# Kernel optimization log

Hardware: AMD Instinct MI355X
Metric: run time of the kernel (lower is better)

## Reference

```python
import jax, jax.numpy as jnp
import numpy as np
import math

B, N, W = 8, 2048, 512

def setup_inputs() -> dict:
    key0 = jax.random.key(0)
    ks = jax.random.split(key0, 6)
    return {
        "query": jax.random.normal(ks[0], (B, N, W), dtype=jnp.float32),
        "key":   jax.random.normal(ks[1], (B, N, W), dtype=jnp.float32),
        "W1": jax.random.normal(ks[2], (W, W), dtype=jnp.float32) * (1.0 / math.sqrt(W)),
        "b1": jax.random.normal(ks[3], (W,), dtype=jnp.float32) * 0.01,
        "W2": jax.random.normal(ks[4], (W, W), dtype=jnp.float32) * (1.0 / math.sqrt(W)),
        "b2": jax.random.normal(ks[5], (W,), dtype=jnp.float32) * 0.01,
    }

def _attn(q, k, v):
    # scores: [B, N, N]
    d_k = q.shape[-1]
    scores = jnp.einsum('bnd,bmd->bnm', q, k) / jnp.sqrt(jnp.asarray(d_k, q.dtype))
    p = jax.nn.softmax(scores, axis=-1)
    return jnp.einsum('bnm,bmd->bnd', p, v)

def reference(query, key, W1, b1, W2, b2):
    # nn.Linear: x @ W.T + b
    q = jnp.einsum('bnd,ed->bne', query, W1) + b1
    k = jnp.einsum('bnd,ed->bne', key, W2) + b2
    x1 = _attn(q, k, q)  # attention(query, key, query)
    x2 = _attn(k, q, k)  # attention(key, query, key)
    return jnp.concatenate((x1, x2), axis=1)  # [B, 2N, W]
```

## Files before the change

kernel.cpp:

```cpp
#include <hip/hip_runtime.h>
#include <hip/hip_bf16.h>
#include <stdint.h>

typedef unsigned short ushort_t;
typedef __attribute__((ext_vector_type(8))) short short8;
typedef __attribute__((ext_vector_type(4))) short short4v;
typedef __attribute__((ext_vector_type(4))) float f32x4;

__device__ inline ushort_t f2bf(float x) {
  uint32_t u = __float_as_uint(x);
  u += 0x7fffu + ((u >> 16) & 1u);
  return (ushort_t)(u >> 16);
}
__device__ inline float bfu2f(uint32_t h) { return __uint_as_float(h << 16); }

__device__ inline uint32_t pk2bf(float a, float b) {
  __hip_bfloat162 h = __float22bfloat162_rn(make_float2(a, b));
  union { __hip_bfloat162 h2; uint32_t u; } cv; cv.h2 = h; return cv.u;
}

__device__ inline void gload_lds16(const void* g, void* l) {
  __builtin_amdgcn_global_load_lds((const __attribute__((address_space(1))) uint32_t*)g,
                                   (__attribute__((address_space(3))) uint32_t*)l, 16, 0, 0);
}

__global__ __launch_bounds__(512, 4) void linear_kernel(
    const float* __restrict__ query, const float* __restrict__ key,
    const float* __restrict__ W1, const float* __restrict__ b1,
    const float* __restrict__ W2, const float* __restrict__ b2,
    ushort_t* __restrict__ q_bf, ushort_t* __restrict__ k_bf,
    ushort_t* __restrict__ qT, ushort_t* __restrict__ kT)
{
  extern __shared__ __attribute__((aligned(16))) ushort_t smL[];

  int bx = blockIdx.x;
  int which = bx & 1, rt = bx >> 1;
  const float* X    = which ? key : query;
  const float* Wm   = which ? W2  : W1;
  const float* bias = which ? b2  : b1;
  ushort_t* OUT  = which ? k_bf : q_bf;
  ushort_t* OUTT = which ? kT   : qT;

  int t = threadIdx.x, w = t >> 6, lane = t & 63, g = lane >> 4, m = lane & 15;

  {
    int tp = t & 127, rsub = t >> 7;
#pragma unroll 4
    for (int p = 0; p < 16; ++p) {
      int row = p * 4 + rsub;
      f32x4 v = *(const f32x4*)(X + (size_t)(rt * 64 + row) * 512 + tp * 4);
      uint2 dv;
      dv.x = pk2bf(v[0], v[1]);
      dv.y = pk2bf(v[2], v[3]);
      int chunk = tp >> 1;
      int phys = chunk ^ (row & 7);
      *(uint2*)&smL[row * 512 + phys * 8 + (tp & 1) * 4] = dv;
    }
  }
  __syncthreads();

  f32x4 zero = {0.f, 0.f, 0.f, 0.f};
  f32x4 acc[4][4];
#pragma unroll
  for (int i = 0; i < 4; ++i)
#pragma unroll
    for (int j = 0; j < 4; ++j) acc[i][j] = zero;

  const float* Wbase = Wm + (size_t)(w * 64) * 512;

  for (int k0 = 0; k0 < 16; ++k0) {
    short8 bfr[4];
#pragma unroll
    for (int j = 0; j < 4; ++j) {
      const float* wp = Wbase + (size_t)(16 * j + m) * 512 + k0 * 32 + g * 8;
      f32x4 lo = *(const f32x4*)wp;
      f32x4 hi = *(const f32x4*)(wp + 4);
      union { uint32_t u[4]; short8 s; } fb;
      fb.u[0] = pk2bf(lo[0], lo[1]); fb.u[1] = pk2bf(lo[2], lo[3]);
      fb.u[2] = pk2bf(hi[0], hi[1]); fb.u[3] = pk2bf(hi[2], hi[3]);
      bfr[j] = fb.s;
    }
    short8 afr[4];
#pragma unroll
    for (int i = 0; i < 4; ++i) {
      int row = 16 * i + m;
      int phys = (k0 * 4 + g) ^ (m & 7);
      afr[i] = *(const short8*)&smL[row * 512 + phys * 8];
    }
#pragma unroll
    for (int i = 0; i < 4; ++i)
#pragma unroll
      for (int j = 0; j < 4; ++j)
        acc[i][j] = __builtin_amdgcn_mfma_f32_16x16x32_bf16(afr[i], bfr[j], acc[i][j], 0, 0, 0);
  }

  float bw[4];
#pragma unroll
  for (int j = 0; j < 4; ++j) bw[j] = bias[w * 64 + 16 * j + m];

  __syncthreads();

#pragma unroll
  for (int j = 0; j < 4; ++j)
#pragma unroll
    for (int i = 0; i < 4; ++i) {
      f32x4 c4 = acc[i][j];
#pragma unroll
      for (int rr = 0; rr < 4; ++rr)
        smL[(16 * i + 4 * g + rr) * 520 + w * 64 + 16 * j + m] = f2bf(c4[rr] + bw[j]);
    }
  __syncthreads();
  {
    int row = t >> 3, oct = t & 7;
    size_t gb = (size_t)(rt * 64 + row) * 512 + oct * 64;
#pragma unroll
    for (int i2 = 0; i2 < 8; ++i2)
      *(short8*)(OUT + gb + i2 * 8) = *(const short8*)&smL[row * 520 + oct * 64 + i2 * 8];
  }
  __syncthreads();

#pragma unroll
  for (int j = 0; j < 4; ++j)
#pragma unroll
    for (int i = 0; i < 4; ++i) {
      f32x4 c4 = acc[i][j];
      short4v tv;
#pragma unroll
      for (int rr = 0; rr < 4; ++rr) tv[rr] = (short)f2bf(c4[rr] + bw[j]);
      *(short4v*)&smL[(w * 64 + 16 * j + m) * 68 + 16 * i + 4 * g] = tv;
    }
  __syncthreads();
  {
    size_t b_ = (size_t)(rt >> 5);
    size_t gb = b_ * (512 * 2048) + (size_t)t * 2048 + (size_t)(rt & 31) * 64;
#pragma unroll
    for (int i2 = 0; i2 < 8; ++i2)
      *(short8*)(OUTT + gb + i2 * 8) = *(const short8*)&smL[t * 68 + i2 * 8];
  }
}

__global__ __launch_bounds__(512, 2) void attn_kernel(
    const ushort_t* __restrict__ qb, const ushort_t* __restrict__ kb_,
    const ushort_t* __restrict__ qT, const ushort_t* __restrict__ kT,
    float* __restrict__ out)
{
  extern __shared__ ushort_t sm[];
  const float CEXP = 1.4426950408889634f / 22.62741699796952f;

  int bx = blockIdx.x;
  int group = bx & 15, mtile = bx >> 4;
  int b = group >> 1, att = group & 1;
  const ushort_t* Qp = (att ? kb_ : qb) + (size_t)b * (2048 * 512);
  const ushort_t* Kp = (att ? qb  : kb_) + (size_t)b * (2048 * 512);
  const ushort_t* Vt = (att ? kT  : qT)  + (size_t)b * (512 * 2048);

  int t = threadIdx.x, w = t >> 6, lane = t & 63, g = lane >> 4, m = lane & 15;
  int dq = w >> 1, qh = w & 1;
  int qrow = mtile * 128 + w * 16 + m;
  int sw8  = ((g ^ ((m >> 1) & 3)) * 8);
  int srow = lane >> 2;
  int soff = ((lane & 3) ^ ((lane >> 3) & 3)) * 8;
  int pm6 = (m & 6);

  ushort_t* Plds = sm + 65536;
  float* lbuf = (float*)(sm + 69632);

  int pw0 = (w * 16 + m) * 32 + ((g ^ pm6) << 2);
  int pw1 = (w * 16 + m) * 32 + (((g + 4) ^ pm6) << 2);
  int prq[4];
#pragma unroll
  for (int qt = 0; qt < 4; ++qt)
    prq[qt] = (qh * 64 + qt * 16 + m) * 32 + (((2 * g) ^ pm6) << 2);

  short8 qf[16];
#pragma unroll
  for (int ks = 0; ks < 16; ++ks)
    qf[ks] = *(const short8*)(Qp + (size_t)qrow * 512 + ks * 32 + g * 8);

  f32x4 zero = {0.f, 0.f, 0.f, 0.f};
  f32x4 acc[8][4];
#pragma unroll
  for (int dt = 0; dt < 8; ++dt)
#pragma unroll
    for (int qt = 0; qt < 4; ++qt) acc[dt][qt] = zero;
  float l = 0.f;

  auto stage = [&](int buf, int kb) {
    ushort_t* base = sm + buf * 32768;
    const int kbase = kb * 32;
#pragma unroll
    for (int i = 0; i < 4; ++i) {
      int qi = w * 4 + i, ks = qi >> 1, tt2 = qi & 1;
      const ushort_t* gsrc = Kp + (size_t)(kbase + tt2 * 16 + srow) * 512 + ks * 32 + soff;
      gload_lds16(gsrc, base + ks * 1024 + tt2 * 512);
    }
#pragma unroll
    for (int i = 0; i < 4; ++i) {
      int qi = w * 4 + i;
      const ushort_t* gsrc = Vt + (size_t)(qi * 16 + srow) * 2048 + kbase + soff;
      gload_lds16(gsrc, base + 16384 + qi * 512);
    }
  };

  stage(0, 0);

  for (int kb = 0; kb < 64; ++kb) {
    int cur = kb & 1;
    __syncthreads();
    if (kb + 1 < 64) stage(1 - cur, kb + 1);
    const ushort_t* base = sm + cur * 32768;

    f32x4 T0 = zero, T1 = zero;
    __builtin_amdgcn_s_setprio(1);
#pragma unroll
    for (int ks = 0; ks < 16; ++ks) {
      short8 k0 = *(const short8*)&base[ks * 1024 +       m * 32 + sw8];
      short8 k1 = *(const short8*)&base[ks * 1024 + 512 + m * 32 + sw8];
      T0 = __builtin_amdgcn_mfma_f32_16x16x32_bf16(k0, qf[ks], T0, 0, 0, 0);
      T1 = __builtin_amdgcn_mfma_f32_16x16x32_bf16(k1, qf[ks], T1, 0, 0, 0);
    }
    __builtin_amdgcn_s_setprio(0);

    uint32_t h[8];
#pragma unroll
    for (int r = 0; r < 4; ++r) {
      float e0 = __builtin_amdgcn_exp2f(T0[r] * CEXP);
      float e1 = __builtin_amdgcn_exp2f(T1[r] * CEXP);
      h[r]     = f2bf(e0);
      h[4 + r] = f2bf(e1);
      l += bfu2f(h[r]) + bfu2f(h[4 + r]);
    }
    uint2 p0, p1;
    p0.x = h[0] | (h[1] << 16); p0.y = h[2] | (h[3] << 16);
    p1.x = h[4] | (h[5] << 16); p1.y = h[6] | (h[7] << 16);
    *(uint2*)&Plds[pw0] = p0;
    *(uint2*)&Plds[pw1] = p1;

    __syncthreads();

    short8 pf[4];
#pragma unroll
    for (int qt = 0; qt < 4; ++qt) pf[qt] = *(const short8*)&Plds[prq[qt]];
    __builtin_amdgcn_s_setprio(1);
#pragma unroll
    for (int dt = 0; dt < 8; ++dt) {
      short8 vf = *(const short8*)&base[16384 + (dq * 8 + dt) * 512 + m * 32 + sw8];
#pragma unroll
      for (int qt = 0; qt < 4; ++qt)
        acc[dt][qt] = __builtin_amdgcn_mfma_f32_16x16x32_bf16(vf, pf[qt], acc[dt][qt], 0, 0, 0);
    }
    __builtin_amdgcn_s_setprio(0);
  }

  l += __shfl_xor(l, 16, 64);
  l += __shfl_xor(l, 32, 64);
  if (lane < 16) lbuf[w * 16 + lane] = 1.0f / l;
  __syncthreads();

  float inv[4];
#pragma unroll
  for (int qt = 0; qt < 4; ++qt) inv[qt] = lbuf[qh * 64 + qt * 16 + m];
  size_t orow = (size_t)b * 4096 + (size_t)att * 2048 + mtile * 128 + qh * 64 + m;
#pragma unroll
  for (int qt = 0; qt < 4; ++qt) {
    float* ob = out + (orow + qt * 16) * 512 + dq * 128;
#pragma unroll
    for (int dt = 0; dt < 8; ++dt) {
      f32x4 v = acc[dt][qt] * inv[qt];
      *(f32x4*)(ob + dt * 16 + g * 4) = v;
    }
  }
}

extern "C" void kernel_launch(void* const* d_in, const int* in_sizes, int n_in,
                              void* d_out, int out_size, void* d_ws, size_t ws_size,
                              hipStream_t stream) {
  const float* query = (const float*)d_in[0];
  const float* key   = (const float*)d_in[1];
  const float* W1    = (const float*)d_in[2];
  const float* b1    = (const float*)d_in[3];
  const float* W2    = (const float*)d_in[4];
  const float* b2    = (const float*)d_in[5];
  float* out = (float*)d_out;

  ushort_t* ws   = (ushort_t*)d_ws;
  ushort_t* q_bf = ws;
  ushort_t* k_bf = ws + 8388608;
  ushort_t* qT   = ws + 16777216;
  ushort_t* kT   = ws + 25165824;

  (void)hipFuncSetAttribute((const void*)linear_kernel,
                            hipFuncAttributeMaxDynamicSharedMemorySize, 69632);
  (void)hipFuncSetAttribute((const void*)attn_kernel,
                            hipFuncAttributeMaxDynamicSharedMemorySize, 139776);

  linear_kernel<<<512, 512, 69632, stream>>>(query, key, W1, b1, W2, b2,
                                             q_bf, k_bf, qT, kT);
  attn_kernel<<<256, 512, 139776, stream>>>(q_bf, k_bf, qT, kT, out);
}
```

Baseline: 331.9 us.

## Pre-convert weights to bf16 and double linear-kernel row tile to 128

Adds a small kernel that converts W1/W2 to bf16 once, so the linear kernel loads bf16 weight fragments directly instead of converting fp32 weights inside every block. The linear kernel now processes 128 rows per block instead of 64, which halves the grid and doubles weight reuse per block at the cost of more accumulator registers and twice the LDS. The bf16 weights are staged in the tail of the output buffer, which the attention kernel later overwrites, so correctness depends on that ordering.

New measurement: 311.9 us. 1.06x faster.

```diff
diff --git a/kernel.cpp b/kernel.cpp
--- a/kernel.cpp
+++ b/kernel.cpp
@@ -24,10 +24,26 @@
                                    (__attribute__((address_space(3))) uint32_t*)l, 16, 0, 0);
 }
 
-__global__ __launch_bounds__(512, 4) void linear_kernel(
+__global__ __launch_bounds__(512) void wcvt_kernel(
+    const float* __restrict__ W1, const float* __restrict__ W2,
+    ushort_t* __restrict__ w1b, ushort_t* __restrict__ w2b)
+{
+  int tid = blockIdx.x * 512 + threadIdx.x;
+  const float* src = (tid < 32768) ? W1 : W2;
+  ushort_t*    dst = (tid < 32768) ? w1b : w2b;
+  int e = (tid & 32767) * 8;
+  f32x4 lo = *(const f32x4*)(src + e);
+  f32x4 hi = *(const f32x4*)(src + e + 4);
+  union { uint32_t u[4]; short8 s; } fb;
+  fb.u[0] = pk2bf(lo[0], lo[1]); fb.u[1] = pk2bf(lo[2], lo[3]);
+  fb.u[2] = pk2bf(hi[0], hi[1]); fb.u[3] = pk2bf(hi[2], hi[3]);
+  *(short8*)(dst + e) = fb.s;
+}
+
+__global__ __launch_bounds__(512, 2) void linear_kernel(
     const float* __restrict__ query, const float* __restrict__ key,
-    const float* __restrict__ W1, const float* __restrict__ b1,
-    const float* __restrict__ W2, const float* __restrict__ b2,
+    const ushort_t* __restrict__ w1b, const float* __restrict__ b1,
+    const ushort_t* __restrict__ w2b, const float* __restrict__ b2,
     ushort_t* __restrict__ q_bf, ushort_t* __restrict__ k_bf,
     ushort_t* __restrict__ qT, ushort_t* __restrict__ kT)
 {
@@ -35,9 +51,9 @@
 
   int bx = blockIdx.x;
   int which = bx & 1, rt = bx >> 1;
-  const float* X    = which ? key : query;
-  const float* Wm   = which ? W2  : W1;
-  const float* bias = which ? b2  : b1;
+  const float* X       = which ? key : query;
+  const ushort_t* Wb   = which ? w2b : w1b;
+  const float* bias    = which ? b2  : b1;
   ushort_t* OUT  = which ? k_bf : q_bf;
   ushort_t* OUTT = which ? kT   : qT;
 
@@ -46,9 +62,9 @@
   {
     int tp = t & 127, rsub = t >> 7;
 #pragma unroll 4
-    for (int p = 0; p < 16; ++p) {
+    for (int p = 0; p < 32; ++p) {
       int row = p * 4 + rsub;
-      f32x4 v = *(const f32x4*)(X + (size_t)(rt * 64 + row) * 512 + tp * 4);
+      f32x4 v = *(const f32x4*)(X + (size_t)(rt * 128 + row) * 512 + tp * 4);
       uint2 dv;
       dv.x = pk2bf(v[0], v[1]);
       dv.y = pk2bf(v[2], v[3]);
@@ -60,35 +76,29 @@
   __syncthreads();
 
   f32x4 zero = {0.f, 0.f, 0.f, 0.f};
-  f32x4 acc[4][4];
-#pragma unroll
-  for (int i = 0; i < 4; ++i)
+  f32x4 acc[8][4];
+#pragma unroll
+  for (int i = 0; i < 8; ++i)
 #pragma unroll
     for (int j = 0; j < 4; ++j) acc[i][j] = zero;
 
-  const float* Wbase = Wm + (size_t)(w * 64) * 512;
-
+  const ushort_t* WbBase = Wb + (size_t)(w * 64) * 512;
+
+#pragma unroll 2
   for (int k0 = 0; k0 < 16; ++k0) {
     short8 bfr[4];
 #pragma unroll
-    for (int j = 0; j < 4; ++j) {
-      const float* wp = Wbase + (size_t)(16 * j + m) * 512 + k0 * 32 + g * 8;
-      f32x4 lo = *(const f32x4*)wp;
-      f32x4 hi = *(const f32x4*)(wp + 4);
-      union { uint32_t u[4]; short8 s; } fb;
-      fb.u[0] = pk2bf(lo[0], lo[1]); fb.u[1] = pk2bf(lo[2], lo[3]);
-      fb.u[2] = pk2bf(hi[0], hi[1]); fb.u[3] = pk2bf(hi[2], hi[3]);
-      bfr[j] = fb.s;
-    }
-    short8 afr[4];
-#pragma unroll
-    for (int i = 0; i < 4; ++i) {
+    for (int j = 0; j < 4; ++j)
+      bfr[j] = *(const short8*)(WbBase + (size_t)(16 * j + m) * 512 + k0 * 32 + g * 8);
+    short8 afr[8];
+#pragma unroll
+    for (int i = 0; i < 8; ++i) {
       int row = 16 * i + m;
       int phys = (k0 * 4 + g) ^ (m & 7);
       afr[i] = *(const short8*)&smL[row * 512 + phys * 8];
     }
 #pragma unroll
-    for (int i = 0; i < 4; ++i)
+    for (int i = 0; i < 8; ++i)
 #pragma unroll
       for (int j = 0; j < 4; ++j)
         acc[i][j] = __builtin_amdgcn_mfma_f32_16x16x32_bf16(afr[i], bfr[j], acc[i][j], 0, 0, 0);
@@ -103,7 +113,7 @@
 #pragma unroll
   for (int j = 0; j < 4; ++j)
 #pragma unroll
-    for (int i = 0; i < 4; ++i) {
+    for (int i = 0; i < 8; ++i) {
       f32x4 c4 = acc[i][j];
 #pragma unroll
       for (int rr = 0; rr < 4; ++rr)
@@ -111,31 +121,31 @@
     }
   __syncthreads();
   {
-    int row = t >> 3, oct = t & 7;
-    size_t gb = (size_t)(rt * 64 + row) * 512 + oct * 64;
-#pragma unroll
-    for (int i2 = 0; i2 < 8; ++i2)
-      *(short8*)(OUT + gb + i2 * 8) = *(const short8*)&smL[row * 520 + oct * 64 + i2 * 8];
+    int row = t >> 2, qtr = t & 3;
+    size_t gb = (size_t)(rt * 128 + row) * 512 + qtr * 128;
+#pragma unroll
+    for (int i2 = 0; i2 < 16; ++i2)
+      *(short8*)(OUT + gb + i2 * 8) = *(const short8*)&smL[row * 520 + qtr * 128 + i2 * 8];
   }
   __syncthreads();
 
 #pragma unroll
   for (int j = 0; j < 4; ++j)
 #pragma unroll
-    for (int i = 0; i < 4; ++i) {
+    for (int i = 0; i < 8; ++i) {
       f32x4 c4 = acc[i][j];
       short4v tv;
 #pragma unroll
       for (int rr = 0; rr < 4; ++rr) tv[rr] = (short)f2bf(c4[rr] + bw[j]);
-      *(short4v*)&smL[(w * 64 + 16 * j + m) * 68 + 16 * i + 4 * g] = tv;
+      *(short4v*)&smL[(w * 64 + 16 * j + m) * 136 + 16 * i + 4 * g] = tv;
     }
   __syncthreads();
   {
-    size_t b_ = (size_t)(rt >> 5);
-    size_t gb = b_ * (512 * 2048) + (size_t)t * 2048 + (size_t)(rt & 31) * 64;
-#pragma unroll
-    for (int i2 = 0; i2 < 8; ++i2)
-      *(short8*)(OUTT + gb + i2 * 8) = *(const short8*)&smL[t * 68 + i2 * 8];
+    size_t b_ = (size_t)(rt >> 4);
+    size_t gb = b_ * (512 * 2048) + (size_t)t * 2048 + (size_t)(rt & 15) * 128;
+#pragma unroll
+    for (int i2 = 0; i2 < 16; ++i2)
+      *(short8*)(OUTT + gb + i2 * 8) = *(const short8*)&smL[t * 136 + i2 * 8];
   }
 }
 
@@ -289,12 +299,16 @@
   ushort_t* qT   = ws + 16777216;
   ushort_t* kT   = ws + 25165824;
 
+  ushort_t* w1b = (ushort_t*)((char*)d_out + 66060288);
+  ushort_t* w2b = w1b + 262144;
+
   (void)hipFuncSetAttribute((const void*)linear_kernel,
-                            hipFuncAttributeMaxDynamicSharedMemorySize, 69632);
+                            hipFuncAttributeMaxDynamicSharedMemorySize, 139264);
   (void)hipFuncSetAttribute((const void*)attn_kernel,
                             hipFuncAttributeMaxDynamicSharedMemorySize, 139776);
 
-  linear_kernel<<<512, 512, 69632, stream>>>(query, key, W1, b1, W2, b2,
-                                             q_bf, k_bf, qT, kT);
+  wcvt_kernel<<<128, 512, 0, stream>>>(W1, W2, w1b, w2b);
+  linear_kernel<<<256, 512, 139264, stream>>>(query, key, w1b, b1, w2b, b2,
+                                              q_bf, k_bf, qT, kT);
   attn_kernel<<<256, 512, 139776, stream>>>(q_bf, k_bf, qT, kT, out);
 }
```
